# Optimization experiments

Hardware: AMD Instinct MI355X
Metric: run time of the kernel (lower is better)

Reference implementation:

```python
import jax, jax.numpy as jnp
import numpy as np

B, N, DIM = 8, 2048, 1024
HEADS, CB_DIM, CB_SIZE = 8, 64, 1024
CB_IN = HEADS * CB_DIM  # 512


def setup_inputs() -> dict:
    key = jax.random.key(0)
    ks = jax.random.split(key, 4)
    x = jax.random.normal(ks[0], (B, N, DIM), dtype=jnp.float32)
    W_in = jax.random.normal(ks[1], (DIM, CB_IN), dtype=jnp.float32) * (DIM ** -0.5)
    b_in = jnp.zeros((CB_IN,), dtype=jnp.float32)
    W_out = jax.random.normal(ks[2], (CB_IN, DIM), dtype=jnp.float32) * (CB_IN ** -0.5)
    b_out = jnp.zeros((DIM,), dtype=jnp.float32)
    embed = jax.random.normal(ks[3], (CB_SIZE, CB_DIM), dtype=jnp.float32)
    return {"x": x, "W_in": W_in, "b_in": b_in, "W_out": W_out, "b_out": b_out, "embed": embed}


def reference(x, W_in, b_in, W_out, b_out, embed):
    # project_in: [B, N, DIM] -> [B, N, HEADS*CB_DIM]
    h = jnp.einsum("bnd,de->bne", x, W_in) + b_in
    # multi-head split, shared codebook: 'b n (h d) -> (b h) n d' view as [B, N, H, d]
    hx = h.reshape(B, N, HEADS, CB_DIM)
    # euclidean nearest neighbor: argmin ||hx - e||^2 == argmax (2 hx.e - ||e||^2)
    dots = jnp.einsum("bnhd,cd->bnhc", hx, embed)          # [B, N, H, C]
    e_sq = jnp.sum(embed * embed, axis=-1)                    # [C]
    scores = 2.0 * dots - e_sq                                 # monotone in -dist
    embed_ind = jnp.argmax(scores, axis=-1)                    # [B, N, H] int
    quantize = embed[embed_ind]                                # [B, N, H, d] gather
    # merge heads and project_out
    q = quantize.reshape(B, N, CB_IN)
    out = jnp.einsum("bne,ed->bnd", q, W_out) + b_out          # [B, N, DIM]
    return out, embed_ind
```

## Files before the change

### kernel.cpp

```cpp
#include <hip/hip_runtime.h>

#define B_      8
#define N_      2048
#define DIM_    1024
#define HEADS_  8
#define CBD_    64
#define CBS_    1024
#define CBIN_   512
#define M_      (B_*N_)
#define M2_     (M_*HEADS_)

#define MARGIN 0.02f
#define XSTR   40

typedef unsigned short ushort_t;
typedef __attribute__((ext_vector_type(8))) short short8;
typedef __attribute__((ext_vector_type(4))) float f32x4;

__device__ inline ushort_t f2bf(float f) {
    unsigned int u = __builtin_bit_cast(unsigned int, f);
    unsigned int r = u + 0x7FFFu + ((u >> 16) & 1u);
    return (ushort_t)(r >> 16);
}
__device__ inline float bf2f(ushort_t h) {
    unsigned int u = ((unsigned int)h) << 16;
    return __builtin_bit_cast(float, u);
}
__device__ inline f32x4 mfma_bf16(short8 a, short8 b, f32x4 c) {
    return __builtin_amdgcn_mfma_f32_16x16x32_bf16(a, b, c, 0, 0, 0);
}
__device__ inline void store4u(ushort_t* p, ushort_t a, ushort_t b, ushort_t c, ushort_t d) {
    uint2 u;
    u.x = (unsigned int)a | ((unsigned int)b << 16);
    u.y = (unsigned int)c | ((unsigned int)d << 16);
    *(uint2*)p = u;
}
__device__ inline void split3(float f, ushort_t& s1, ushort_t& s2, ushort_t& s3) {
    s1 = f2bf(f);
    float r = f - bf2f(s1);
    s2 = f2bf(r);
    float r2 = r - bf2f(s2);
    s3 = f2bf(r2);
}

__global__ __launch_bounds__(256) void esq_kernel(const float* __restrict__ embed,
                                                  float* __restrict__ esq) {
    int c = blockIdx.x * 256 + threadIdx.x;
    if (c < CBS_) {
        const float* e = embed + (size_t)c * CBD_;
        float s = 0.f;
#pragma unroll
        for (int d = 0; d < CBD_; ++d) s += e[d] * e[d];
        esq[c] = s;
    }
}

__global__ __launch_bounds__(256) void split_embed(const float* __restrict__ embed,
                                                   ushort_t* __restrict__ hi,
                                                   ushort_t* __restrict__ lo) {
    int i = blockIdx.x * 256 + threadIdx.x;
    float f = embed[i];
    ushort_t h = f2bf(f);
    hi[i] = h;
    lo[i] = f2bf(f - bf2f(h));
}

__global__ __launch_bounds__(256) void transposeW(const float* __restrict__ W,
                                                  ushort_t* __restrict__ WT) {
    __shared__ ushort_t t[64][65];
    const int tid = threadIdx.x;
    const int n0 = blockIdx.x * 64, k0 = blockIdx.y * 64;
#pragma unroll
    for (int s = 0; s < 16; ++s) {
        int i = s * 256 + tid;
        int r = i >> 6, c = i & 63;
        t[r][c] = f2bf(W[(size_t)(k0 + r) * DIM_ + n0 + c]);
    }
    __syncthreads();
#pragma unroll
    for (int s = 0; s < 16; ++s) {
        int i = s * 256 + tid;
        int r = i >> 6, c = i & 63;
        WT[(size_t)(n0 + r) * CBIN_ + k0 + c] = t[c][r];
    }
}

__global__ __launch_bounds__(256) void split_WinT(const float* __restrict__ W,
                                                  ushort_t* __restrict__ W1T,
                                                  ushort_t* __restrict__ W2T,
                                                  ushort_t* __restrict__ W3T) {
    __shared__ ushort_t t1[64][65];
    __shared__ ushort_t t2[64][65];
    __shared__ ushort_t t3[64][65];
    const int tid = threadIdx.x;
    const int n0 = blockIdx.x * 64, k0 = blockIdx.y * 64;
#pragma unroll
    for (int s = 0; s < 16; ++s) {
        int i = s * 256 + tid;
        int r = i >> 6, c = i & 63;
        float f = W[(size_t)(k0 + r) * CBIN_ + n0 + c];
        split3(f, t1[r][c], t2[r][c], t3[r][c]);
    }
    __syncthreads();
#pragma unroll
    for (int s = 0; s < 16; ++s) {
        int i = s * 256 + tid;
        int r = i >> 6, c = i & 63;
        size_t o = (size_t)(n0 + r) * DIM_ + k0 + c;
        W1T[o] = t1[c][r];
        W2T[o] = t2[c][r];
        W3T[o] = t3[c][r];
    }
}

__global__ __launch_bounds__(256) void gemm_in_x6(const float* __restrict__ x,
                                                  const ushort_t* __restrict__ W1T,
                                                  const ushort_t* __restrict__ W2T,
                                                  const ushort_t* __restrict__ W3T,
                                                  const float* __restrict__ bias,
                                                  float* __restrict__ C) {
    __shared__ ushort_t A1[128 * XSTR];
    __shared__ ushort_t A2[128 * XSTR];
    __shared__ ushort_t A3[128 * XSTR];
    __shared__ ushort_t B1[128 * XSTR];
    __shared__ ushort_t B2[128 * XSTR];
    __shared__ ushort_t B3[128 * XSTR];

    const int tid  = threadIdx.x;
    const int lane = tid & 63;
    const int w    = tid >> 6;
    const int quad = lane >> 4;
    const int col  = lane & 15;
    const int m0   = blockIdx.y * 128;
    const int n0   = blockIdx.x * 128;
    const int wm   = (w & 1) * 64;
    const int wn   = (w >> 1) * 64;

    f32x4 acc[4][4];
#pragma unroll
    for (int rt = 0; rt < 4; ++rt)
#pragma unroll
        for (int ct = 0; ct < 4; ++ct) acc[rt][ct] = (f32x4){0.f, 0.f, 0.f, 0.f};

    for (int k0 = 0; k0 < DIM_; k0 += 32) {
        __syncthreads();
#pragma unroll
        for (int s = 0; s < 4; ++s) {
            int f = s * 256 + tid;
            int row = f >> 3, qq = f & 7;
            float4 v = *(const float4*)(x + (size_t)(m0 + row) * DIM_ + k0 + qq * 4);
            float vv[4] = {v.x, v.y, v.z, v.w};
            ushort_t p1[4], p2[4], p3[4];
#pragma unroll
            for (int j = 0; j < 4; ++j) split3(vv[j], p1[j], p2[j], p3[j]);
            int base = row * XSTR + qq * 4;
            store4u(&A1[base], p1[0], p1[1], p1[2], p1[3]);
            store4u(&A2[base], p2[0], p2[1], p2[2], p2[3]);
            store4u(&A3[base], p3[0], p3[1], p3[2], p3[3]);
        }
#pragma unroll
        for (int s = 0; s < 2; ++s) {
            int f = s * 256 + tid;
            int row = f >> 2, g = f & 3;
            size_t go = (size_t)(n0 + row) * DIM_ + k0 + g * 8;
            int lo = row * XSTR + g * 8;
            *(uint4*)&B1[lo] = *(const uint4*)(W1T + go);
            *(uint4*)&B2[lo] = *(const uint4*)(W2T + go);
            *(uint4*)&B3[lo] = *(const uint4*)(W3T + go);
        }
        __syncthreads();

        short8 a1[4], a2[4], a3[4], b1[4], b2[4], b3[4];
#pragma unroll
        for (int rt = 0; rt < 4; ++rt) {
            int o = (wm + rt * 16 + col) * XSTR + quad * 8;
            a1[rt] = *(const short8*)&A1[o];
            a2[rt] = *(const short8*)&A2[o];
            a3[rt] = *(const short8*)&A3[o];
        }
#pragma unroll
        for (int ct = 0; ct < 4; ++ct) {
            int o = (wn + ct * 16 + col) * XSTR + quad * 8;
            b1[ct] = *(const short8*)&B1[o];
            b2[ct] = *(const short8*)&B2[o];
            b3[ct] = *(const short8*)&B3[o];
        }
#define COMBO(AP, BP)                                                   \
        _Pragma("unroll")                                               \
        for (int ct = 0; ct < 4; ++ct)                                  \
            _Pragma("unroll")                                           \
            for (int rt = 0; rt < 4; ++rt)                              \
                acc[rt][ct] = mfma_bf16(AP[rt], BP[ct], acc[rt][ct]);
        COMBO(a1, b1); COMBO(a1, b2); COMBO(a2, b1);
        COMBO(a2, b2); COMBO(a1, b3); COMBO(a3, b1);
#undef COMBO
    }

#pragma unroll
    for (int ct = 0; ct < 4; ++ct) {
        int gc = n0 + wn + ct * 16 + col;
        float bb = bias[gc];
#pragma unroll
        for (int rt = 0; rt < 4; ++rt) {
#pragma unroll
            for (int reg = 0; reg < 4; ++reg) {
                int gr = m0 + wm + rt * 16 + quad * 4 + reg;
                C[(size_t)gr * CBIN_ + gc] = acc[rt][ct][reg] + bb;
            }
        }
    }
}

__global__ __launch_bounds__(256) void argmax2(const float* __restrict__ h,
                                               const ushort_t* __restrict__ embhi,
                                               const ushort_t* __restrict__ emblo,
                                               const float* __restrict__ esq,
                                               const float* __restrict__ embed,
                                               float* __restrict__ outIdxF,
                                               int* __restrict__ outIdxI) {
    __shared__ ushort_t HXHI[128 * 72];
    __shared__ ushort_t HXLO[128 * 72];
    __shared__ ushort_t EBHI[64 * 72];
    __shared__ ushort_t EBLO[64 * 72];
    __shared__ float    ESQ[CBS_];
    __shared__ int      BIDX[128];
    __shared__ int      FLAG[128];
    __shared__ int      NFLAG;

    const int tid  = threadIdx.x;
    const int lane = tid & 63;
    const int w    = tid >> 6;
    const int quad = lane >> 4;
    const int col  = lane & 15;
    const int r0   = blockIdx.x * 128;

    if (tid == 0) NFLAG = 0;

#pragma unroll
    for (int s = 0; s < 8; ++s) {
        int f = s * 256 + tid;
        int row = f >> 4, q = f & 15;
        float4 v = *(const float4*)(h + (size_t)(r0 + row) * 64 + q * 4);
        float vv[4] = {v.x, v.y, v.z, v.w};
        ushort_t hi[4], lo[4];
#pragma unroll
        for (int j = 0; j < 4; ++j) {
            hi[j] = f2bf(vv[j]);
            lo[j] = f2bf(vv[j] - bf2f(hi[j]));
        }
        int base = row * 72 + q * 4;
        store4u(&HXHI[base], hi[0], hi[1], hi[2], hi[3]);
        store4u(&HXLO[base], lo[0], lo[1], lo[2], lo[3]);
    }
    *(float4*)&ESQ[tid * 4] = *(const float4*)(esq + tid * 4);
    __syncthreads();

    short8 AH[2][2], AL[2][2];
#pragma unroll
    for (int rt = 0; rt < 2; ++rt)
#pragma unroll
        for (int ks = 0; ks < 2; ++ks) {
            int m = w * 32 + rt * 16 + col;
            int offs = m * 72 + ks * 32 + quad * 8;
            AH[rt][ks] = *(const short8*)&HXHI[offs];
            AL[rt][ks] = *(const short8*)&HXLO[offs];
        }

    float v1[8], v2[8];
    int   i1[8];
#pragma unroll
    for (int s = 0; s < 8; ++s) { v1[s] = -3.4e38f; v2[s] = -3.4e38f; i1[s] = 0; }

    for (int ch = 0; ch < 16; ++ch) {
        __syncthreads();
#pragma unroll
        for (int s = 0; s < 2; ++s) {
            int f = s * 256 + tid;
            int row = f >> 3, g = f & 7;
            *(uint4*)&EBHI[row * 72 + g * 8] =
                *(const uint4*)(embhi + (size_t)(ch * 64 + row) * 64 + g * 8);
            *(uint4*)&EBLO[row * 72 + g * 8] =
                *(const uint4*)(emblo + (size_t)(ch * 64 + row) * 64 + g * 8);
        }
        __syncthreads();
#pragma unroll
        for (int ct = 0; ct < 4; ++ct) {
            int nb = (ct * 16 + col) * 72 + quad * 8;
            short8 BH0 = *(const short8*)&EBHI[nb];
            short8 BH1 = *(const short8*)&EBHI[nb + 32];
            short8 BL0 = *(const short8*)&EBLO[nb];
            short8 BL1 = *(const short8*)&EBLO[nb + 32];
            int code = ch * 64 + ct * 16 + col;
            float eq = ESQ[code];
#pragma unroll
            for (int rt = 0; rt < 2; ++rt) {
                f32x4 acc = {0.f, 0.f, 0.f, 0.f};
                acc = mfma_bf16(AH[rt][0], BH0, acc);
                acc = mfma_bf16(AH[rt][1], BH1, acc);
                acc = mfma_bf16(AH[rt][0], BL0, acc);
                acc = mfma_bf16(AH[rt][1], BL1, acc);
                acc = mfma_bf16(AL[rt][0], BH0, acc);
                acc = mfma_bf16(AL[rt][1], BH1, acc);
#pragma unroll
                for (int reg = 0; reg < 4; ++reg) {
                    int st = rt * 4 + reg;
                    float sc = fmaf(2.f, acc[reg], -eq);
                    float losr = fminf(sc, v1[st]);
                    v2[st] = fmaxf(v2[st], losr);
                    bool gt = sc > v1[st];
                    v1[st] = fmaxf(v1[st], sc);
                    i1[st] = gt ? code : i1[st];
                }
            }
        }
    }

#pragma unroll
    for (int st = 0; st < 8; ++st) {
#pragma unroll
        for (int m = 1; m <= 8; m <<= 1) {
            float ov1 = __shfl_xor(v1[st], m);
            int   oi1 = __shfl_xor(i1[st], m);
            float ov2 = __shfl_xor(v2[st], m);
            float losr = fminf(v1[st], ov1);
            v2[st] = fmaxf(fmaxf(v2[st], ov2), losr);
            bool take = (ov1 > v1[st]) || (ov1 == v1[st] && oi1 < i1[st]);
            v1[st] = take ? ov1 : v1[st];
            i1[st] = take ? oi1 : i1[st];
        }
        if (col == 0) {
            int rt = st >> 2, reg = st & 3;
            int row_l = w * 32 + rt * 16 + quad * 4 + reg;
            BIDX[row_l] = i1[st];
            if (v1[st] - v2[st] < MARGIN) {
                int p = atomicAdd(&NFLAG, 1);
                FLAG[p] = row_l;
            }
        }
    }
    __syncthreads();

    int nf = NFLAG;
    for (int i = w; i < nf; i += 4) {
        int row_l = FLAG[i];
        const float* hr = h + (size_t)(r0 + row_l) * 64;
        float accf[16];
#pragma unroll
        for (int j = 0; j < 16; ++j) accf[j] = 0.f;
        for (int d4 = 0; d4 < 16; ++d4) {
            float4 hv = *(const float4*)(hr + d4 * 4);
#pragma unroll
            for (int j = 0; j < 16; ++j) {
                int c = lane + 64 * j;
                float4 ev = *(const float4*)(embed + (size_t)c * 64 + d4 * 4);
                accf[j] += hv.x * ev.x + hv.y * ev.y + hv.z * ev.z + hv.w * ev.w;
            }
        }
        float best = -3.4e38f; int bi = 0;
#pragma unroll
        for (int j = 0; j < 16; ++j) {
            int c = lane + 64 * j;
            float sc = 2.f * accf[j] - ESQ[c];
            if (sc > best) { best = sc; bi = c; }
        }
#pragma unroll
        for (int m = 1; m <= 32; m <<= 1) {
            float ob = __shfl_xor(best, m);
            int  obi = __shfl_xor(bi, m);
            if (ob > best || (ob == best && obi < bi)) { best = ob; bi = obi; }
        }
        if (lane == 0) BIDX[row_l] = bi;
    }
    __syncthreads();

    if (tid < 128) {
        int b = BIDX[tid];
        outIdxF[r0 + tid] = (float)b;
        outIdxI[r0 + tid] = b;
    }
}

__global__ __launch_bounds__(256) void gemm_out_bf16(const ushort_t* __restrict__ embhi,
                                                     const int* __restrict__ idx,
                                                     const ushort_t* __restrict__ WbfT,
                                                     const float* __restrict__ bias,
                                                     float* __restrict__ C) {
    __shared__ ushort_t Qs[128 * 72];
    __shared__ ushort_t Ws[128 * 72];
    __shared__ int idxs[128 * HEADS_];

    const int tid  = threadIdx.x;
    const int lane = tid & 63;
    const int w    = tid >> 6;
    const int quad = lane >> 4;
    const int col  = lane & 15;
    const int m0   = blockIdx.y * 128;
    const int n0   = blockIdx.x * 128;
    const int wm   = (w & 1) * 64;
    const int wn   = (w >> 1) * 64;

#pragma unroll
    for (int s = 0; s < 4; ++s) {
        int f = s * 256 + tid;
        idxs[f] = idx[(size_t)m0 * HEADS_ + f];
    }

    f32x4 acc[4][4];
#pragma unroll
    for (int rt = 0; rt < 4; ++rt)
#pragma unroll
        for (int ct = 0; ct < 4; ++ct) acc[rt][ct] = (f32x4){0.f, 0.f, 0.f, 0.f};

    for (int k0 = 0; k0 < CBIN_; k0 += 64) {
        __syncthreads();
        int head = k0 >> 6;
#pragma unroll
        for (int s = 0; s < 4; ++s) {
            int f = s * 256 + tid;
            int row = f >> 3, g = f & 7;
            int e = idxs[row * HEADS_ + head];
            *(uint4*)&Qs[row * 72 + g * 8] = *(const uint4*)(embhi + (size_t)e * 64 + g * 8);
            *(uint4*)&Ws[row * 72 + g * 8] =
                *(const uint4*)(WbfT + (size_t)(n0 + row) * CBIN_ + k0 + g * 8);
        }
        __syncthreads();
#pragma unroll
        for (int ks = 0; ks < 2; ++ks) {
            short8 a[4], b[4];
#pragma unroll
            for (int rt = 0; rt < 4; ++rt)
                a[rt] = *(const short8*)&Qs[(wm + rt * 16 + col) * 72 + ks * 32 + quad * 8];
#pragma unroll
            for (int ct = 0; ct < 4; ++ct)
                b[ct] = *(const short8*)&Ws[(wn + ct * 16 + col) * 72 + ks * 32 + quad * 8];
#pragma unroll
            for (int rt = 0; rt < 4; ++rt)
#pragma unroll
                for (int ct = 0; ct < 4; ++ct)
                    acc[rt][ct] = mfma_bf16(a[rt], b[ct], acc[rt][ct]);
        }
    }

#pragma unroll
    for (int ct = 0; ct < 4; ++ct) {
        int gc = n0 + wn + ct * 16 + col;
        float bb = bias[gc];
#pragma unroll
        for (int rt = 0; rt < 4; ++rt) {
#pragma unroll
            for (int reg = 0; reg < 4; ++reg) {
                int gr = m0 + wm + rt * 16 + quad * 4 + reg;
                C[(size_t)gr * DIM_ + gc] = acc[rt][ct][reg] + bb;
            }
        }
    }
}

extern "C" void kernel_launch(void* const* d_in, const int* in_sizes, int n_in,
                              void* d_out, int out_size, void* d_ws, size_t ws_size,
                              hipStream_t stream) {
    const float* x     = (const float*)d_in[0];
    const float* W_in  = (const float*)d_in[1];
    const float* b_in  = (const float*)d_in[2];
    const float* W_out = (const float*)d_in[3];
    const float* b_out = (const float*)d_in[4];
    const float* embed = (const float*)d_in[5];

    float* out     = (float*)d_out;
    float* outIdxF = out + (size_t)M_ * DIM_;

    char* ws = (char*)d_ws;
    float*    h     = (float*)ws;
    int*      idxI  = (int*)(ws + 33554432);
    float*    esq   = (float*)(ws + 34078720);
    ushort_t* embhi = (ushort_t*)(ws + 34082816);
    ushort_t* emblo = (ushort_t*)(ws + 34213888);
    ushort_t* WbfT  = (ushort_t*)(ws + 34344960);
    ushort_t* W1T   = (ushort_t*)(ws + 35393536);
    ushort_t* W2T   = (ushort_t*)(ws + 36442112);
    ushort_t* W3T   = (ushort_t*)(ws + 37490688);

    esq_kernel<<<dim3(CBS_ / 256), dim3(256), 0, stream>>>(embed, esq);
    split_embed<<<dim3(CBS_ * CBD_ / 256), dim3(256), 0, stream>>>(embed, embhi, emblo);
    transposeW<<<dim3(DIM_ / 64, CBIN_ / 64), dim3(256), 0, stream>>>(W_out, WbfT);
    split_WinT<<<dim3(CBIN_ / 64, DIM_ / 64), dim3(256), 0, stream>>>(W_in, W1T, W2T, W3T);
    gemm_in_x6<<<dim3(CBIN_ / 128, M_ / 128), dim3(256), 0, stream>>>(x, W1T, W2T, W3T,
                                                                      b_in, h);
    argmax2<<<dim3(M2_ / 128), dim3(256), 0, stream>>>(h, embhi, emblo, esq, embed,
                                                       outIdxF, idxI);
    gemm_out_bf16<<<dim3(DIM_ / 128, M_ / 128), dim3(256), 0, stream>>>(embhi, idxI, WbfT,
                                                                        b_out, out);
}
```

Before: 377.0 us.

## Load codebook and activations directly from global memory in argmax kernel

The argmax kernel no longer stages the activation tile, codebook chunks and squared norms through shared memory. Each lane loads its MFMA operand fragments straight from global memory (relying on L1/L2 caching of the small codebook) and does the hi/lo bf16 split in registers. This removes per-chunk __syncthreads barriers and cuts LDS usage, which may raise occupancy, but adds uncoalesced, redundant global loads. It also unrolls the chunk loop by two and folds the second-best update into a single fmed3 instruction.

```diff
diff --git a/kernel.cpp b/kernel.cpp
--- a/kernel.cpp
+++ b/kernel.cpp
@@ -218,14 +218,9 @@
                                                const float* __restrict__ embed,
                                                float* __restrict__ outIdxF,
                                                int* __restrict__ outIdxI) {
-    __shared__ ushort_t HXHI[128 * 72];
-    __shared__ ushort_t HXLO[128 * 72];
-    __shared__ ushort_t EBHI[64 * 72];
-    __shared__ ushort_t EBLO[64 * 72];
-    __shared__ float    ESQ[CBS_];
-    __shared__ int      BIDX[128];
-    __shared__ int      FLAG[128];
-    __shared__ int      NFLAG;
+    __shared__ int BIDX[128];
+    __shared__ int FLAG[128];
+    __shared__ int NFLAG;
 
     const int tid  = threadIdx.x;
     const int lane = tid & 63;
@@ -235,63 +230,46 @@
     const int r0   = blockIdx.x * 128;
 
     if (tid == 0) NFLAG = 0;
-
-#pragma unroll
-    for (int s = 0; s < 8; ++s) {
-        int f = s * 256 + tid;
-        int row = f >> 4, q = f & 15;
-        float4 v = *(const float4*)(h + (size_t)(r0 + row) * 64 + q * 4);
-        float vv[4] = {v.x, v.y, v.z, v.w};
-        ushort_t hi[4], lo[4];
-#pragma unroll
-        for (int j = 0; j < 4; ++j) {
-            hi[j] = f2bf(vv[j]);
-            lo[j] = f2bf(vv[j] - bf2f(hi[j]));
-        }
-        int base = row * 72 + q * 4;
-        store4u(&HXHI[base], hi[0], hi[1], hi[2], hi[3]);
-        store4u(&HXLO[base], lo[0], lo[1], lo[2], lo[3]);
-    }
-    *(float4*)&ESQ[tid * 4] = *(const float4*)(esq + tid * 4);
     __syncthreads();
 
     short8 AH[2][2], AL[2][2];
 #pragma unroll
-    for (int rt = 0; rt < 2; ++rt)
+    for (int rt = 0; rt < 2; ++rt) {
+        const float* hp = h + (size_t)(r0 + w * 32 + rt * 16 + col) * 64 + quad * 8;
 #pragma unroll
         for (int ks = 0; ks < 2; ++ks) {
-            int m = w * 32 + rt * 16 + col;
-            int offs = m * 72 + ks * 32 + quad * 8;
-            AH[rt][ks] = *(const short8*)&HXHI[offs];
-            AL[rt][ks] = *(const short8*)&HXLO[offs];
-        }
+            float4 u0 = *(const float4*)(hp + ks * 32);
+            float4 u1 = *(const float4*)(hp + ks * 32 + 4);
+            float vv[8] = {u0.x, u0.y, u0.z, u0.w, u1.x, u1.y, u1.z, u1.w};
+            short8 hh, ll;
+#pragma unroll
+            for (int j = 0; j < 8; ++j) {
+                ushort_t hi = f2bf(vv[j]);
+                hh[j] = (short)hi;
+                ll[j] = (short)f2bf(vv[j] - bf2f(hi));
+            }
+            AH[rt][ks] = hh;
+            AL[rt][ks] = ll;
+        }
+    }
 
     float v1[8], v2[8];
     int   i1[8];
 #pragma unroll
     for (int s = 0; s < 8; ++s) { v1[s] = -3.4e38f; v2[s] = -3.4e38f; i1[s] = 0; }
 
+#pragma unroll 2
     for (int ch = 0; ch < 16; ++ch) {
-        __syncthreads();
-#pragma unroll
-        for (int s = 0; s < 2; ++s) {
-            int f = s * 256 + tid;
-            int row = f >> 3, g = f & 7;
-            *(uint4*)&EBHI[row * 72 + g * 8] =
-                *(const uint4*)(embhi + (size_t)(ch * 64 + row) * 64 + g * 8);
-            *(uint4*)&EBLO[row * 72 + g * 8] =
-                *(const uint4*)(emblo + (size_t)(ch * 64 + row) * 64 + g * 8);
-        }
-        __syncthreads();
 #pragma unroll
         for (int ct = 0; ct < 4; ++ct) {
-            int nb = (ct * 16 + col) * 72 + quad * 8;
-            short8 BH0 = *(const short8*)&EBHI[nb];
-            short8 BH1 = *(const short8*)&EBHI[nb + 32];
-            short8 BL0 = *(const short8*)&EBLO[nb];
-            short8 BL1 = *(const short8*)&EBLO[nb + 32];
-            int code = ch * 64 + ct * 16 + col;
-            float eq = ESQ[code];
+            const int code = ch * 64 + ct * 16 + col;
+            const ushort_t* eh = embhi + (size_t)code * 64 + quad * 8;
+            const ushort_t* el = emblo + (size_t)code * 64 + quad * 8;
+            short8 BH0 = *(const short8*)eh;
+            short8 BH1 = *(const short8*)(eh + 32);
+            short8 BL0 = *(const short8*)el;
+            short8 BL1 = *(const short8*)(el + 32);
+            float eq = esq[code];
 #pragma unroll
             for (int rt = 0; rt < 2; ++rt) {
                 f32x4 acc = {0.f, 0.f, 0.f, 0.f};
@@ -303,10 +281,9 @@
                 acc = mfma_bf16(AL[rt][1], BH1, acc);
 #pragma unroll
                 for (int reg = 0; reg < 4; ++reg) {
-                    int st = rt * 4 + reg;
+                    const int st = rt * 4 + reg;
                     float sc = fmaf(2.f, acc[reg], -eq);
-                    float losr = fminf(sc, v1[st]);
-                    v2[st] = fmaxf(v2[st], losr);
+                    v2[st] = __builtin_amdgcn_fmed3f(sc, v1[st], v2[st]);
                     bool gt = sc > v1[st];
                     v1[st] = fmaxf(v1[st], sc);
                     i1[st] = gt ? code : i1[st];
@@ -360,7 +337,7 @@
 #pragma unroll
         for (int j = 0; j < 16; ++j) {
             int c = lane + 64 * j;
-            float sc = 2.f * accf[j] - ESQ[c];
+            float sc = 2.f * accf[j] - esq[c];
             if (sc > best) { best = sc; bi = c; }
         }
 #pragma unroll
```

Result: slower. 462.4 us (+22.7%).
